# Performance work log

Measured on AMD Instinct MI355X. Metric: run time of the kernel, lower is better.

The kernel has to match this reference:

```python
import math
import jax, jax.numpy as jnp
import numpy as np

N, T, D, H, DH = 4, 2048, 1024, 16, 64
CAP = 30.0
EPS = 1e-5


def _layernorm(x, g, b):
    m = jnp.mean(x, axis=-1, keepdims=True)
    v = jnp.mean(jnp.square(x - m), axis=-1, keepdims=True)
    return (x - m) * jax.lax.rsqrt(v + EPS) * g + b


def _rope(x):
    # x: [N, H, t, d]; interleaved rotary (rotary-embedding-torch style), theta=10000
    t, d = x.shape[2], x.shape[3]
    inv_freq = 1.0 / (10000.0 ** (jnp.arange(0, d, 2, dtype=jnp.float32) / d))
    ang = jnp.arange(t, dtype=jnp.float32)[:, None] * inv_freq[None, :]  # [t, d/2]
    cos, sin = jnp.cos(ang), jnp.sin(ang)
    x1, x2 = x[..., 0::2], x[..., 1::2]
    r1 = x1 * cos - x2 * sin
    r2 = x1 * sin + x2 * cos
    return jnp.stack([r1, r2], axis=-1).reshape(x.shape)


def setup_inputs() -> dict:
    key = jax.random.key(0)
    ks = jax.random.split(key, 8)
    s = 0.02
    lengths = jax.random.randint(ks[6], (N,), T // 2, T + 1).astype(jnp.int32)
    key_padding_mask = jnp.arange(T)[None, :] >= lengths[:, None]  # True = pad
    attn_mask = jnp.triu(jnp.ones((T, T), dtype=bool), 1)  # causal: True = masked
    return {
        "x": jax.random.normal(ks[0], (N, T, D), jnp.float32),
        "ln_g": jnp.ones((D,), jnp.float32),
        "ln_b": jnp.zeros((D,), jnp.float32),
        "Wq": jax.random.normal(ks[1], (D, H * DH), jnp.float32) * s,
        "bq": jnp.zeros((H * DH,), jnp.float32),
        "Wk": jax.random.normal(ks[2], (D, H * DH), jnp.float32) * s,
        "bk": jnp.zeros((H * DH,), jnp.float32),
        "Wv": jax.random.normal(ks[3], (D, H * DH), jnp.float32) * s,
        "bv": jnp.zeros((H * DH,), jnp.float32),
        "Wo": jax.random.normal(ks[4], (H * DH, D), jnp.float32) * s,
        "bo": jnp.zeros((D,), jnp.float32),
        "key_padding_mask": key_padding_mask,
        "attn_mask": attn_mask,
        "key_value_sequence_lengths": lengths,
    }


def reference(x, ln_g, ln_b, Wq, bq, Wk, bk, Wv, bv, Wo, bo,
              key_padding_mask, attn_mask, key_value_sequence_lengths):
    n, t, _ = x.shape
    h = _layernorm(x, ln_g, ln_b)  # shared LN for q/k/v (self-attention)
    q = (h @ Wq + bq).reshape(n, t, H, DH).transpose(0, 2, 1, 3)  # [n,H,t,d]
    k = (h @ Wk + bk).reshape(n, t, H, DH).transpose(0, 2, 1, 3)
    v = (h @ Wv + bv).reshape(n, t, H, DH).transpose(0, 2, 1, 3)
    q = _rope(q)
    k = _rope(k)
    scores = jnp.einsum('bhtd,bhTd->bhtT', q, k) / math.sqrt(DH)
    scores = CAP * jnp.tanh(scores / CAP)  # tanh soft-cap
    mask = key_padding_mask[:, None, None, :] | attn_mask[None, None, :, :]
    scores = jnp.where(mask, -jnp.inf, scores)
    attn = jax.nn.softmax(scores, axis=-1)
    out = jnp.einsum('bhtT,bhTd->bhtd', attn, v)
    out = out.transpose(0, 2, 1, 3).reshape(n, t, H * DH)
    return out @ Wo + bo
```

## Files before the change

kernel.cpp:

```cpp
#include <hip/hip_runtime.h>
#include <hip/hip_bf16.h>

typedef unsigned short u16;
typedef unsigned int   u32;
typedef __bf16 bf16x8 __attribute__((ext_vector_type(8)));
typedef float  f32x4  __attribute__((ext_vector_type(4)));

#define NB 4
#define T_ 2048
#define D_ 1024
#define H_ 16
#define DH 64
#define M_ (NB * T_)
#define PSTR 72

__device__ __forceinline__ float bf2f(u16 u) {
    union { u32 i; float f; } v; v.i = ((u32)u) << 16; return v.f;
}
__device__ __forceinline__ u16 f2bf(float f) {
    union { float fl; u32 i; } v; v.fl = f;
    u32 r = v.i + 0x7fff + ((v.i >> 16) & 1);
    return (u16)(r >> 16);
}

__device__ __forceinline__ void gl_lds16(const u16* g, u16* l) {
    __builtin_amdgcn_global_load_lds((const __attribute__((address_space(1))) void*)g,
                                     (__attribute__((address_space(3))) void*)l,
                                     16, 0, 0);
}

__device__ __forceinline__ int detect_f32(const u16* p) {
    int weird = 0;
    const int lane = threadIdx.x & 63;
    #pragma unroll
    for (int i = 0; i < 4; ++i) {
        const u16 u = p[lane * 4 + i];
        const int e = (u >> 7) & 0xFF;
        weird += (e == 0xFF || (e >= 0x01 && e <= 0x3F) || (e >= 0xC0 && e <= 0xFE));
    }
    #pragma unroll
    for (int off = 32; off; off >>= 1) weird += __shfl_xor(weird, off);
    return weird >= 16;
}

__device__ __forceinline__ int read_len(const void* raw, int b) {
    const int* a32 = (const int*)raw;
    bool ok32 = true;
    #pragma unroll
    for (int i = 0; i < NB; ++i) {
        const int v = a32[i];
        if (v < 1 || v > T_) ok32 = false;
    }
    int v = ok32 ? a32[b] : (int)((const long long*)raw)[b];
    return min(max(v, 1), T_);
}

__global__ __launch_bounds__(256) void prep_kernel(const void* __restrict__ xraw,
                                                   const void* __restrict__ graw,
                                                   const void* __restrict__ braw,
                                                   u16* __restrict__ h,
                                                   const void* __restrict__ W0,
                                                   const void* __restrict__ W1,
                                                   const void* __restrict__ W2,
                                                   const void* __restrict__ W3,
                                                   u16* __restrict__ Wt0,
                                                   u16* __restrict__ Wt1,
                                                   u16* __restrict__ Wt2,
                                                   u16* __restrict__ Wt3,
                                                   float2* __restrict__ tab) {
    __shared__ __align__(16) u16 sh[64 * PSTR];
    const int bid = blockIdx.x;
    const int tid = threadIdx.x;

    if (bid < M_) {
        const int row = bid;
        const int isf = detect_f32((const u16*)xraw);
        float* red = (float*)sh;

        float xv[4];
        if (isf) {
            const float* xr = (const float*)xraw + (size_t)row * D_;
            *(float4*)xv = *(const float4*)&xr[tid * 4];
        } else {
            const u16* xr = (const u16*)xraw + (size_t)row * D_;
            u16 loc[4] __attribute__((aligned(8)));
            *(uint2*)loc = *(const uint2*)&xr[tid * 4];
            #pragma unroll
            for (int i = 0; i < 4; ++i) xv[i] = bf2f(loc[i]);
        }

        float s = xv[0] + xv[1] + xv[2] + xv[3];
        float q = xv[0]*xv[0] + xv[1]*xv[1] + xv[2]*xv[2] + xv[3]*xv[3];
        #pragma unroll
        for (int off = 32; off; off >>= 1) {
            s += __shfl_xor(s, off);
            q += __shfl_xor(q, off);
        }
        const int wave = tid >> 6, lane = tid & 63;
        if (lane == 0) { red[wave] = s; red[4 + wave] = q; }
        __syncthreads();
        s = red[0] + red[1] + red[2] + red[3];
        q = red[4] + red[5] + red[6] + red[7];

        const float mean = s * (1.0f / D_);
        const float var  = q * (1.0f / D_) - mean * mean;
        const float rs   = rsqrtf(var + 1e-5f);

        u16 o[4] __attribute__((aligned(8)));
        #pragma unroll
        for (int i = 0; i < 4; ++i) {
            const int c = tid * 4 + i;
            const float gv = isf ? ((const float*)graw)[c] : bf2f(((const u16*)graw)[c]);
            const float bv = isf ? ((const float*)braw)[c] : bf2f(((const u16*)braw)[c]);
            o[i] = f2bf((xv[i] - mean) * rs * gv + bv);
        }
        *(uint2*)&h[(size_t)row * D_ + tid * 4] = *(uint2*)o;
    } else if (bid < M_ + 1024) {
        const int w = bid - M_;
        const int z = w >> 8;
        const int t = w & 255;
        const void* Wraw = (z == 0) ? W0 : (z == 1) ? W1 : (z == 2) ? W2 : W3;
        u16* Wt          = (z == 0) ? Wt0 : (z == 1) ? Wt1 : (z == 2) ? Wt2 : Wt3;
        u16 (*tile)[PSTR] = (u16(*)[PSTR])sh;
        const int isf = detect_f32((const u16*)Wraw);
        const int n0 = (t & 15) * 64;
        const int k0 = (t >> 4) * 64;
        const int tr  = tid >> 2;
        const int tc  = (tid & 3) * 16;

        if (isf) {
            const float* W = (const float*)Wraw;
            #pragma unroll
            for (int i = 0; i < 16; ++i)
                tile[tc + i][tr] = f2bf(W[(size_t)(k0 + tr) * D_ + n0 + tc + i]);
        } else {
            const u16* W = (const u16*)Wraw;
            #pragma unroll
            for (int i = 0; i < 16; ++i)
                tile[tc + i][tr] = W[(size_t)(k0 + tr) * D_ + n0 + tc + i];
        }
        __syncthreads();
        *(uint4*)&Wt[(size_t)(n0 + tr) * D_ + k0 + tc]     = *(uint4*)&tile[tr][tc];
        *(uint4*)&Wt[(size_t)(n0 + tr) * D_ + k0 + tc + 8] = *(uint4*)&tile[tr][tc + 8];
    } else {
        const int gid = (bid - (M_ + 1024)) * 256 + tid;
        const int t = gid >> 5, i = gid & 31;
        const float inv = exp2f(-(float)i * 0.41524101186092f);
        const float ang = (float)t * inv;
        float sv, cv;
        sincosf(ang, &sv, &cv);
        tab[gid] = make_float2(cv, sv);
    }
}

__global__ __launch_bounds__(256) void wconv_kernel(const void* __restrict__ Wraw,
                                                    u16* __restrict__ Wt) {
    __shared__ u16 tile[64][PSTR];
    const int isf = detect_f32((const u16*)Wraw);
    const int n0 = blockIdx.x * 64;
    const int k0 = blockIdx.y * 64;
    const int tid = threadIdx.x;
    const int tr  = tid >> 2;
    const int tc  = (tid & 3) * 16;

    if (isf) {
        const float* W = (const float*)Wraw;
        #pragma unroll
        for (int i = 0; i < 16; ++i)
            tile[tc + i][tr] = f2bf(W[(size_t)(k0 + tr) * D_ + n0 + tc + i]);
    } else {
        const u16* W = (const u16*)Wraw;
        #pragma unroll
        for (int i = 0; i < 16; ++i)
            tile[tc + i][tr] = W[(size_t)(k0 + tr) * D_ + n0 + tc + i];
    }
    __syncthreads();
    *(uint4*)&Wt[(size_t)(n0 + tr) * D_ + k0 + tc]     = *(uint4*)&tile[tr][tc];
    *(uint4*)&Wt[(size_t)(n0 + tr) * D_ + k0 + tc + 8] = *(uint4*)&tile[tr][tc + 8];
}

__global__ __launch_bounds__(256) void vtrans_kernel(const u16* __restrict__ vtmp,
                                                     u16* __restrict__ vt) {
    __shared__ u16 tile[64][PSTR];
    const int bh = blockIdx.y;
    const int b  = bh >> 4;
    const int hh = bh & 15;
    const int t0 = blockIdx.x * 64;
    const int tid = threadIdx.x;
    const int tr  = tid >> 2;
    const int tc  = (tid & 3) * 16;

    #pragma unroll
    for (int i = 0; i < 16; ++i)
        tile[tc + i][tr] = vtmp[(size_t)(b * T_ + t0 + tr) * D_ + hh * DH + tc + i];
    __syncthreads();
    u16* dst = vt + (size_t)bh * DH * T_ + (size_t)tr * T_ + t0;
    *(uint4*)&dst[tc]     = *(uint4*)&tile[tr][tc];
    *(uint4*)&dst[tc + 8] = *(uint4*)&tile[tr][tc + 8];
}

__global__ __launch_bounds__(256) void qkv_kernel(const u16* __restrict__ A,
                                                  const u16* __restrict__ Wt3,
                                                  const void* __restrict__ Braw,
                                                  const void* __restrict__ bqr,
                                                  const void* __restrict__ bkr,
                                                  const void* __restrict__ bvr,
                                                  u16* __restrict__ qo,
                                                  u16* __restrict__ ko,
                                                  u16* __restrict__ vo,
                                                  const float2* __restrict__ tab) {
    __shared__ __align__(16) u16 As[128 * 64];
    __shared__ __align__(16) u16 Bs[128 * 64];

    const int tid   = threadIdx.x;
    const int wave  = tid >> 6;
    const int lane  = tid & 63;
    const int quad  = lane >> 4;
    const int lr    = lane & 15;

    const int bid = blockIdx.x;
    const int wg  = (bid & 7) * 192 + (bid >> 3);
    const int ntile = (wg % 24) * 128;
    const int mtile = (wg / 24) * 128;
    const int seg   = ntile >> 10;

    const int isf = detect_f32((const u16*)Braw);

    const int srow = wave * 8 + (lane >> 3);
    const int sc   = (((lane & 7) ^ (lane >> 3)) * 8);
    const u16* aP = A   + (size_t)(mtile + srow) * D_ + sc;
    const u16* bP = Wt3 + (size_t)(ntile + srow) * D_ + sc;
    u16* aL = As + (wave * 8) * 64;
    u16* bL = Bs + (wave * 8) * 64;

    const int mbase = (wave >> 1) * 64;
    const int nbase = (wave & 1) * 64;

    f32x4 acc[4][4];
    #pragma unroll
    for (int m = 0; m < 4; ++m)
        #pragma unroll
        for (int n = 0; n < 4; ++n)
            acc[m][n] = (f32x4){0.f, 0.f, 0.f, 0.f};

    for (int k0 = 0; k0 < D_; k0 += 64) {
        #pragma unroll
        for (int j = 0; j < 4; ++j) {
            gl_lds16(aP + (size_t)(j * 32) * D_ + k0, aL + (j * 32) * 64);
            gl_lds16(bP + (size_t)(j * 32) * D_ + k0, bL + (j * 32) * 64);
        }
        __syncthreads();

        #pragma unroll
        for (int c = 0; c < 2; ++c) {
            bf16x8 af[4], bfr[4];
            #pragma unroll
            for (int m = 0; m < 4; ++m) {
                const int row = mbase + m * 16 + lr;
                af[m] = *(const bf16x8*)&As[row * 64 + (((c << 2) | quad) ^ (row & 7)) * 8];
            }
            #pragma unroll
            for (int n = 0; n < 4; ++n) {
                const int row = nbase + n * 16 + lr;
                bfr[n] = *(const bf16x8*)&Bs[row * 64 + (((c << 2) | quad) ^ (row & 7)) * 8];
            }
            #pragma unroll
            for (int m = 0; m < 4; ++m)
                #pragma unroll
                for (int n = 0; n < 4; ++n)
                    acc[m][n] = __builtin_amdgcn_mfma_f32_16x16x32_bf16(af[m], bfr[n], acc[m][n], 0, 0, 0);
        }
        __syncthreads();
    }

    const void* biasraw = (seg == 0) ? bqr : (seg == 1) ? bkr : bvr;
    u16* out            = (seg == 0) ? qo  : (seg == 1) ? ko  : vo;
    const int nloc = (ntile & 1023) + nbase;

    #pragma unroll
    for (int m = 0; m < 4; ++m) {
        #pragma unroll
        for (int n = 0; n < 4; ++n) {
            const int ncl = nloc + n * 16 + lr;
            const float bv = isf ? ((const float*)biasraw)[ncl]
                                 : bf2f(((const u16*)biasraw)[ncl]);
            #pragma unroll
            for (int r = 0; r < 4; ++r) {
                const int mrow = mtile + mbase + m * 16 + quad * 4 + r;
                float v = acc[m][n][r] + bv;
                if (seg < 2) {
                    const float other = __shfl_xor(v, 1);
                    const int d = ncl & (DH - 1);
                    const int t = mrow & (T_ - 1);
                    const float2 cs = tab[t * 32 + (d >> 1)];
                    v = (d & 1) ? (other * cs.y + v * cs.x) : (v * cs.x - other * cs.y);
                }
                out[(size_t)mrow * D_ + ncl] = f2bf(v);
            }
        }
    }
}

__global__ __launch_bounds__(256) void gemm128_kernel(const u16* __restrict__ A,
                                                      const u16* __restrict__ Bt,
                                                      const void* __restrict__ Braw,
                                                      const void* __restrict__ biasraw,
                                                      void* __restrict__ out,
                                                      const int nx,
                                                      const int mode) {
    __shared__ __align__(16) u16 As[128 * 64];
    __shared__ __align__(16) u16 Bs[128 * 64];

    const int tid   = threadIdx.x;
    const int wave  = tid >> 6;
    const int lane  = tid & 63;
    const int quad  = lane >> 4;
    const int lr    = lane & 15;

    const int bid = blockIdx.x;
    const int cpx = (nx * (M_ / 128)) >> 3;
    const int wg  = (bid & 7) * cpx + (bid >> 3);
    const int ntile = (wg % nx) * 128;
    const int mtile = (wg / nx) * 128;

    const int isf = detect_f32((const u16*)Braw);

    const int srow = wave * 8 + (lane >> 3);
    const int sc   = (((lane & 7) ^ (lane >> 3)) * 8);
    const u16* aP = A  + (size_t)(mtile + srow) * D_ + sc;
    const u16* bP = Bt + (size_t)(ntile + srow) * D_ + sc;
    u16* aL = As + (wave * 8) * 64;
    u16* bL = Bs + (wave * 8) * 64;

    const int mbase = (wave >> 1) * 64;
    const int nbase = (wave & 1) * 64;

    f32x4 acc[4][4];
    #pragma unroll
    for (int m = 0; m < 4; ++m)
        #pragma unroll
        for (int n = 0; n < 4; ++n)
            acc[m][n] = (f32x4){0.f, 0.f, 0.f, 0.f};

    for (int k0 = 0; k0 < D_; k0 += 64) {
        #pragma unroll
        for (int j = 0; j < 4; ++j) {
            gl_lds16(aP + (size_t)(j * 32) * D_ + k0, aL + (j * 32) * 64);
            gl_lds16(bP + (size_t)(j * 32) * D_ + k0, bL + (j * 32) * 64);
        }
        __syncthreads();

        #pragma unroll
        for (int c = 0; c < 2; ++c) {
            bf16x8 af[4], bfr[4];
            #pragma unroll
            for (int m = 0; m < 4; ++m) {
                const int row = mbase + m * 16 + lr;
                af[m] = *(const bf16x8*)&As[row * 64 + (((c << 2) | quad) ^ (row & 7)) * 8];
            }
            #pragma unroll
            for (int n = 0; n < 4; ++n) {
                const int row = nbase + n * 16 + lr;
                bfr[n] = *(const bf16x8*)&Bs[row * 64 + (((c << 2) | quad) ^ (row & 7)) * 8];
            }
            #pragma unroll
            for (int m = 0; m < 4; ++m)
                #pragma unroll
                for (int n = 0; n < 4; ++n)
                    acc[m][n] = __builtin_amdgcn_mfma_f32_16x16x32_bf16(af[m], bfr[n], acc[m][n], 0, 0, 0);
        }
        __syncthreads();
    }

    #pragma unroll
    for (int m = 0; m < 4; ++m) {
        #pragma unroll
        for (int n = 0; n < 4; ++n) {
            const int ncol = ntile + nbase + n * 16 + lr;
            const float bv = isf ? ((const float*)biasraw)[ncol]
                                 : bf2f(((const u16*)biasraw)[ncol]);
            #pragma unroll
            for (int r = 0; r < 4; ++r) {
                const int mrow = mtile + mbase + m * 16 + quad * 4 + r;
                float v = acc[m][n][r] + bv;
                if (mode == 2) {
                    const float other = __shfl_xor(v, 1);
                    const int d = ncol & (DH - 1);
                    const int t = mrow & (T_ - 1);
                    const int i = d >> 1;
                    const float inv = exp2f(-(float)i * 0.41524101186092f);
                    const float ang = (float)t * inv;
                    float sv, cv;
                    __sincosf(ang, &sv, &cv);
                    v = (d & 1) ? (other * sv + v * cv) : (v * cv - other * sv);
                }
                const int d  = ncol & (DH - 1);
                const int hh = ncol >> 6;
                const int t  = mrow & (T_ - 1);
                const int bb = mrow >> 11;
                if (mode == 0) {
                    if (isf) ((float*)out)[(size_t)mrow * D_ + ncol] = v;
                    else     ((u16*)out)[(size_t)mrow * D_ + ncol] = f2bf(v);
                } else if (mode == 1) {
                    ((u16*)out)[(((size_t)(bb * H_ + hh) * DH) + d) * T_ + t] = f2bf(v);
                } else {
                    ((u16*)out)[(((size_t)(bb * H_ + hh) * T_) + t) * DH + d] = f2bf(v);
                }
            }
        }
    }
}

__global__ __launch_bounds__(256) void gemm_kernel(const u16* __restrict__ A,
                                                   const void* __restrict__ Braw,
                                                   const void* __restrict__ biasraw,
                                                   void* __restrict__ out,
                                                   const int mode) {
    __shared__ __align__(16) u16 As[128 * 32];
    __shared__ __align__(16) u16 Bs[64 * 32];

    const int tid   = threadIdx.x;
    const int ntile = blockIdx.x * 64;
    const int mtile = blockIdx.y * 128;
    const int wave  = tid >> 6;
    const int lane  = tid & 63;
    const int quad  = lane >> 4;
    const int lr    = lane & 15;

    const int isf = detect_f32((const u16*)Braw);
    const float* Bf = (const float*)Braw;
    const u16*   Bu = (const u16*)Braw;

    f32x4 acc[2][4];
    #pragma unroll
    for (int s = 0; s < 2; ++s)
        #pragma unroll
        for (int n = 0; n < 4; ++n)
            acc[s][n] = (f32x4){0.f, 0.f, 0.f, 0.f};

    const int ar  = tid >> 1;
    const int akb = (tid & 1) * 16;
    const int bn  = tid & 63;
    const int bkb = (tid >> 6) * 8;
    const u16* Arow = A + (size_t)(mtile + ar) * D_ + akb;
    const size_t bcol0 = (size_t)bkb * D_ + ntile + bn;

    for (int k0 = 0; k0 < D_; k0 += 32) {
        *(uint4*)&As[ar * 32 + akb]     = *(const uint4*)(Arow + k0);
        *(uint4*)&As[ar * 32 + akb + 8] = *(const uint4*)(Arow + k0 + 8);
        {
            u16 tmp[8] __attribute__((aligned(16)));
            if (isf) {
                #pragma unroll
                for (int j = 0; j < 8; ++j) tmp[j] = f2bf(Bf[bcol0 + (size_t)(k0 + j) * D_]);
            } else {
                #pragma unroll
                for (int j = 0; j < 8; ++j) tmp[j] = Bu[bcol0 + (size_t)(k0 + j) * D_];
            }
            *(uint4*)&Bs[bn * 32 + bkb] = *(uint4*)tmp;
        }
        __syncthreads();

        const int mbase = wave * 32;
        bf16x8 af0 = *(const bf16x8*)&As[(mbase +      lr) * 32 + quad * 8];
        bf16x8 af1 = *(const bf16x8*)&As[(mbase + 16 + lr) * 32 + quad * 8];
        #pragma unroll
        for (int nt = 0; nt < 4; ++nt) {
            bf16x8 bf = *(const bf16x8*)&Bs[(nt * 16 + lr) * 32 + quad * 8];
            acc[0][nt] = __builtin_amdgcn_mfma_f32_16x16x32_bf16(af0, bf, acc[0][nt], 0, 0, 0);
            acc[1][nt] = __builtin_amdgcn_mfma_f32_16x16x32_bf16(af1, bf, acc[1][nt], 0, 0, 0);
        }
        __syncthreads();
    }

    #pragma unroll
    for (int s2 = 0; s2 < 2; ++s2) {
        #pragma unroll
        for (int nt = 0; nt < 4; ++nt) {
            const int ncol = ntile + nt * 16 + lr;
            const float bv = isf ? ((const float*)biasraw)[ncol]
                                 : bf2f(((const u16*)biasraw)[ncol]);
            #pragma unroll
            for (int r = 0; r < 4; ++r) {
                const int mrow = mtile + wave * 32 + s2 * 16 + quad * 4 + r;
                float v = acc[s2][nt][r] + bv;
                if (mode == 2) {
                    const float other = __shfl_xor(v, 1);
                    const int d = ncol & (DH - 1);
                    const int t = mrow & (T_ - 1);
                    const int i = d >> 1;
                    const float inv = exp2f(-(float)i * 0.41524101186092f);
                    const float ang = (float)t * inv;
                    const float cv = cosf(ang), sv = sinf(ang);
                    v = (d & 1) ? (other * sv + v * cv) : (v * cv - other * sv);
                }
                const int d  = ncol & (DH - 1);
                const int hh = ncol >> 6;
                const int t  = mrow & (T_ - 1);
                const int bb = mrow >> 11;
                if (mode == 0) {
                    if (isf) ((float*)out)[(size_t)mrow * D_ + ncol] = v;
                    else     ((u16*)out)[(size_t)mrow * D_ + ncol] = f2bf(v);
                } else if (mode == 1) {
                    ((u16*)out)[(((size_t)(bb * H_ + hh) * DH) + d) * T_ + t] = f2bf(v);
                } else {
                    ((u16*)out)[(((size_t)(bb * H_ + hh) * T_) + t) * DH + d] = f2bf(v);
                }
            }
        }
    }
}

__global__ __launch_bounds__(256) void attn_kernel(const u16* __restrict__ Q,
                                                   const u16* __restrict__ K,
                                                   const u16* __restrict__ Vt,
                                                   const void* __restrict__ lensraw,
                                                   u16* __restrict__ ctx,
                                                   const int rowmajor) {
    __shared__ __align__(16) u16 Ps[64 * PSTR];
    __shared__ __align__(16) u16 Ps2[64 * PSTR];
    __shared__ __align__(16) u16 Ks[64 * PSTR];
    __shared__ __align__(16) u16 Vts[64 * PSTR];

    const int tid  = threadIdx.x;
    const int wave = tid >> 6;
    const int lane = tid & 63;
    const int quad = lane >> 4;
    const int lr   = lane & 15;

    const int bid = blockIdx.x;
    const int swz = (bid & 7) * 128 + (bid >> 3);
    const int qx  = swz & 15;
    const int bh  = swz >> 4;
    const int qs_lo = qx * 64;
    const int qs_hi = (31 - qx) * 64;
    const int b    = bh >> 4;
    const int hh   = bh & 15;
    const int len  = read_len(lensraw, b);

    const size_t qkstride = rowmajor ? (size_t)D_ : (size_t)DH;
    const size_t qkoff    = rowmajor ? ((size_t)b * T_ * D_ + hh * DH)
                                     : ((size_t)bh * T_ * DH);
    const u16* Qp = Q + qkoff;
    const u16* Kp = K + qkoff;
    const u16* Vb = Vt + (size_t)bh * DH * T_;

    const int srow = tid >> 2;
    const int scb  = (tid & 3) * 16;

    *(uint4*)&Ps[srow * PSTR + scb]     = *(const uint4*)&Qp[(size_t)(qs_lo + srow) * qkstride + scb];
    *(uint4*)&Ps[srow * PSTR + scb + 8] = *(const uint4*)&Qp[(size_t)(qs_lo + srow) * qkstride + scb + 8];
    const bf16x8 qaL0 = *(const bf16x8*)&Ps[(wave * 16 + lr) * PSTR + quad * 8];
    const bf16x8 qaL1 = *(const bf16x8*)&Ps[(wave * 16 + lr) * PSTR + 32 + quad * 8];
    *(uint4*)&Ps[srow * PSTR + scb]     = *(const uint4*)&Qp[(size_t)(qs_hi + srow) * qkstride + scb];
    *(uint4*)&Ps[srow * PSTR + scb + 8] = *(const uint4*)&Qp[(size_t)(qs_hi + srow) * qkstride + scb + 8];
    const bf16x8 qaH0 = *(const bf16x8*)&Ps[(wave * 16 + lr) * PSTR + quad * 8];
    const bf16x8 qaH1 = *(const bf16x8*)&Ps[(wave * 16 + lr) * PSTR + 32 + quad * 8];

    {
        uint4 k0 = *(const uint4*)&Kp[(size_t)srow * qkstride + scb];
        uint4 k1 = *(const uint4*)&Kp[(size_t)srow * qkstride + scb + 8];
        uint4 v0 = *(const uint4*)&Vb[(size_t)srow * T_ + scb];
        uint4 v1 = *(const uint4*)&Vb[(size_t)srow * T_ + scb + 8];
        *(uint4*)&Ks[srow * PSTR + scb]      = k0;
        *(uint4*)&Ks[srow * PSTR + scb + 8]  = k1;
        *(uint4*)&Vts[srow * PSTR + scb]     = v0;
        *(uint4*)&Vts[srow * PSTR + scb + 8] = v1;
    }
    __syncthreads();

    f32x4 accL[4], accH[4];
    float lL[4] = {0.f, 0.f, 0.f, 0.f};
    float lH[4] = {0.f, 0.f, 0.f, 0.f};
    #pragma unroll
    for (int nt = 0; nt < 4; ++nt) {
        accL[nt] = (f32x4){0.f, 0.f, 0.f, 0.f};
        accH[nt] = (f32x4){0.f, 0.f, 0.f, 0.f};
    }

    const int ktnL = min(qs_lo + 63, len - 1) / 64 + 1;
    const int ktnH = min(qs_hi + 63, len - 1) / 64 + 1;
    const int prow = wave * 16 + quad * 4;

    const float C1 = 1.44269504f / 120.0f;
    const float C2 = -60.0f * 1.44269504f;

    uint4 kr0, kr1, vr0, vr1;
    for (int kt = 0; kt < ktnH; ++kt) {
        const int ks = kt * 64;
        const bool havenext = (kt + 1 < ktnH);
        const bool lo_act   = (kt < ktnL);

        if (havenext) {
            const int ns = ks + 64;
            kr0 = *(const uint4*)&Kp[(size_t)(ns + srow) * qkstride + scb];
            kr1 = *(const uint4*)&Kp[(size_t)(ns + srow) * qkstride + scb + 8];
            vr0 = *(const uint4*)&Vb[(size_t)srow * T_ + ns + scb];
            vr1 = *(const uint4*)&Vb[(size_t)srow * T_ + ns + scb + 8];
        }

        f32x4 sH[4], sL[4];
        #pragma unroll
        for (int nt = 0; nt < 4; ++nt) {
            sH[nt] = (f32x4){0.f, 0.f, 0.f, 0.f};
            sL[nt] = (f32x4){0.f, 0.f, 0.f, 0.f};
        }
        __builtin_amdgcn_s_setprio(1);
        #pragma unroll
        for (int nt = 0; nt < 4; ++nt) {
            bf16x8 kb0 = *(const bf16x8*)&Ks[(nt * 16 + lr) * PSTR + quad * 8];
            bf16x8 kb1 = *(const bf16x8*)&Ks[(nt * 16 + lr) * PSTR + 32 + quad * 8];
            sH[nt] = __builtin_amdgcn_mfma_f32_16x16x32_bf16(qaH0, kb0, sH[nt], 0, 0, 0);
            sH[nt] = __builtin_amdgcn_mfma_f32_16x16x32_bf16(qaH1, kb1, sH[nt], 0, 0, 0);
            if (lo_act) {
                sL[nt] = __builtin_amdgcn_mfma_f32_16x16x32_bf16(qaL0, kb0, sL[nt], 0, 0, 0);
                sL[nt] = __builtin_amdgcn_mfma_f32_16x16x32_bf16(qaL1, kb1, sL[nt], 0, 0, 0);
            }
        }
        __builtin_amdgcn_s_setprio(0);

        {
            const bool mH = (ks == qs_hi) || (ks + 63 >= len);
            if (!mH) {
                #pragma unroll
                for (int r = 0; r < 4; ++r) {
                    #pragma unroll
                    for (int nt = 0; nt < 4; ++nt) {
                        const float z = __builtin_amdgcn_exp2f(sH[nt][r] * C1);
                        const float p = __builtin_amdgcn_exp2f(C2 * __builtin_amdgcn_rcpf(z + 1.0f));
                        lH[r] += p;
                        Ps[(prow + r) * PSTR + nt * 16 + lr] = f2bf(p);
                    }
                }
            } else {
                #pragma unroll
                for (int r = 0; r < 4; ++r) {
                    const int trow = qs_hi + prow + r;
                    #pragma unroll
                    for (int nt = 0; nt < 4; ++nt) {
                        const float z = __builtin_amdgcn_exp2f(sH[nt][r] * C1);
                        float p = __builtin_amdgcn_exp2f(C2 * __builtin_amdgcn_rcpf(z + 1.0f));
                        const int col = ks + nt * 16 + lr;
                        p = (col > trow || col >= len) ? 0.f : p;
                        lH[r] += p;
                        Ps[(prow + r) * PSTR + nt * 16 + lr] = f2bf(p);
                    }
                }
            }
        }
        if (lo_act) {
            const bool mL = (ks == qs_lo) || (ks + 63 >= len);
            if (!mL) {
                #pragma unroll
                for (int r = 0; r < 4; ++r) {
                    #pragma unroll
                    for (int nt = 0; nt < 4; ++nt) {
                        const float z = __builtin_amdgcn_exp2f(sL[nt][r] * C1);
                        const float p = __builtin_amdgcn_exp2f(C2 * __builtin_amdgcn_rcpf(z + 1.0f));
                        lL[r] += p;
                        Ps2[(prow + r) * PSTR + nt * 16 + lr] = f2bf(p);
                    }
                }
            } else {
                #pragma unroll
                for (int r = 0; r < 4; ++r) {
                    const int trow = qs_lo + prow + r;
                    #pragma unroll
                    for (int nt = 0; nt < 4; ++nt) {
                        const float z = __builtin_amdgcn_exp2f(sL[nt][r] * C1);
                        float p = __builtin_amdgcn_exp2f(C2 * __builtin_amdgcn_rcpf(z + 1.0f));
                        const int col = ks + nt * 16 + lr;
                        p = (col > trow || col >= len) ? 0.f : p;
                        lL[r] += p;
                        Ps2[(prow + r) * PSTR + nt * 16 + lr] = f2bf(p);
                    }
                }
            }
        }

        bf16x8 paH0 = *(const bf16x8*)&Ps[(wave * 16 + lr) * PSTR + quad * 8];
        bf16x8 paH1 = *(const bf16x8*)&Ps[(wave * 16 + lr) * PSTR + 32 + quad * 8];
        bf16x8 paL0 = *(const bf16x8*)&Ps2[(wave * 16 + lr) * PSTR + quad * 8];
        bf16x8 paL1 = *(const bf16x8*)&Ps2[(wave * 16 + lr) * PSTR + 32 + quad * 8];
        __builtin_amdgcn_s_setprio(1);
        #pragma unroll
        for (int nt = 0; nt < 4; ++nt) {
            bf16x8 vb0 = *(const bf16x8*)&Vts[(nt * 16 + lr) * PSTR + quad * 8];
            bf16x8 vb1 = *(const bf16x8*)&Vts[(nt * 16 + lr) * PSTR + 32 + quad * 8];
            accH[nt] = __builtin_amdgcn_mfma_f32_16x16x32_bf16(paH0, vb0, accH[nt], 0, 0, 0);
            accH[nt] = __builtin_amdgcn_mfma_f32_16x16x32_bf16(paH1, vb1, accH[nt], 0, 0, 0);
            if (lo_act) {
                accL[nt] = __builtin_amdgcn_mfma_f32_16x16x32_bf16(paL0, vb0, accL[nt], 0, 0, 0);
                accL[nt] = __builtin_amdgcn_mfma_f32_16x16x32_bf16(paL1, vb1, accL[nt], 0, 0, 0);
            }
        }
        __builtin_amdgcn_s_setprio(0);

        if (havenext) {
            __syncthreads();
            *(uint4*)&Ks[srow * PSTR + scb]      = kr0;
            *(uint4*)&Ks[srow * PSTR + scb + 8]  = kr1;
            *(uint4*)&Vts[srow * PSTR + scb]     = vr0;
            *(uint4*)&Vts[srow * PSTR + scb + 8] = vr1;
            __syncthreads();
        }
    }

    #pragma unroll
    for (int r = 0; r < 4; ++r) {
        float ll = lL[r], lh = lH[r];
        #pragma unroll
        for (int off = 1; off < 16; off <<= 1) {
            ll += __shfl_xor(ll, off);
            lh += __shfl_xor(lh, off);
        }
        const float invL = (ll > 0.f) ? (1.0f / ll) : 0.f;
        const float invH = (lh > 0.f) ? (1.0f / lh) : 0.f;
        const int qrow = prow + r;
        #pragma unroll
        for (int nt = 0; nt < 4; ++nt) {
            ctx[(size_t)(b * T_ + qs_lo + qrow) * D_ + hh * DH + nt * 16 + lr] =
                f2bf(accL[nt][r] * invL);
            ctx[(size_t)(b * T_ + qs_hi + qrow) * D_ + hh * DH + nt * 16 + lr] =
                f2bf(accH[nt][r] * invH);
        }
    }
}

extern "C" void kernel_launch(void* const* d_in, const int* in_sizes, int n_in,
                              void* d_out, int out_size, void* d_ws, size_t ws_size,
                              hipStream_t stream) {
    u16* h = (u16*)d_ws;
    const size_t MD = (size_t)M_ * D_;
    const size_t WD = (size_t)D_ * D_;
    u16* q  = h + MD;
    u16* k  = q + MD;
    u16* vt = k + MD;
    const bool havewt  = ws_size >= (4 * MD + 4 * WD) * sizeof(u16);
    const bool havebig = ws_size >= (5 * MD + 4 * WD) * sizeof(u16)
                                    + (size_t)T_ * 32 * sizeof(float2);
    u16* wtq = havewt ? (vt + MD)  : nullptr;
    u16* wtk = havewt ? (wtq + WD) : nullptr;
    u16* wtv = havewt ? (wtk + WD) : nullptr;
    u16* wto = havewt ? (wtv + WD) : nullptr;
    u16* vtmp = havebig ? (wto + WD) : nullptr;
    float2* tab = havebig ? (float2*)(vtmp + MD) : nullptr;

    if (havebig) {
        prep_kernel<<<M_ + 1024 + 256, 256, 0, stream>>>(
            d_in[0], d_in[1], d_in[2], h,
            d_in[3], d_in[5], d_in[7], d_in[9], wtq, wtk, wtv, wto, tab);

        qkv_kernel<<<1536, 256, 0, stream>>>(
            h, wtq, d_in[3], d_in[4], d_in[6], d_in[8], q, k, vtmp, tab);

        vtrans_kernel<<<dim3(T_ / 64, NB * H_), 256, 0, stream>>>(vtmp, vt);

        attn_kernel<<<(T_ / 128) * NB * H_, 256, 0, stream>>>(q, k, vt, d_in[13], h, 1);

        gemm128_kernel<<<8 * (M_ / 128), 256, 0, stream>>>(
            h, wto, d_in[9], d_in[10], d_out, 8, 0);
    } else if (havewt) {
        prep_kernel<<<M_, 256, 0, stream>>>(
            d_in[0], d_in[1], d_in[2], h,
            d_in[3], d_in[5], d_in[7], d_in[9], wtq, wtk, wtv, wto, nullptr);
        dim3 wgrid(D_ / 64, D_ / 64);
        wconv_kernel<<<wgrid, 256, 0, stream>>>(d_in[3], wtq);
        wconv_kernel<<<wgrid, 256, 0, stream>>>(d_in[5], wtk);
        wconv_kernel<<<wgrid, 256, 0, stream>>>(d_in[7], wtv);
        wconv_kernel<<<wgrid, 256, 0, stream>>>(d_in[9], wto);

        const int g1 = 8 * (M_ / 128);
        gemm128_kernel<<<g1, 256, 0, stream>>>(h, wtq, d_in[3], d_in[4], q, 8, 2);
        gemm128_kernel<<<g1, 256, 0, stream>>>(h, wtk, d_in[5], d_in[6], k, 8, 2);
        gemm128_kernel<<<g1, 256, 0, stream>>>(h, wtv, d_in[7], d_in[8], vt, 8, 1);

        attn_kernel<<<(T_ / 128) * NB * H_, 256, 0, stream>>>(q, k, vt, d_in[13], h, 0);

        gemm128_kernel<<<g1, 256, 0, stream>>>(h, wto, d_in[9], d_in[10], d_out, 8, 0);
    } else {
        prep_kernel<<<M_, 256, 0, stream>>>(
            d_in[0], d_in[1], d_in[2], h,
            d_in[3], d_in[5], d_in[7], d_in[9], nullptr, nullptr, nullptr, nullptr, nullptr);
        dim3 ggrid(D_ / 64, M_ / 128);
        gemm_kernel<<<ggrid, 256, 0, stream>>>(h, d_in[3], d_in[4], q, 2);
        gemm_kernel<<<ggrid, 256, 0, stream>>>(h, d_in[5], d_in[6], k, 2);
        gemm_kernel<<<ggrid, 256, 0, stream>>>(h, d_in[7], d_in[8], vt, 1);

        attn_kernel<<<(T_ / 128) * NB * H_, 256, 0, stream>>>(q, k, vt, d_in[13], h, 0);

        gemm_kernel<<<ggrid, 256, 0, stream>>>(h, d_in[9], d_in[10], d_out, 0);
    }
}
```

Measured before the change: 381.4 us.

## Replace paired-tile causal attention with persistent atomic work queue ordered longest-first

The attention kernel no longer pairs a low and high query tile per block to balance causal work. It now runs a persistent grid of 1024 blocks that pull single 64-row query tiles from a global atomic counter, in order from longest (highest query tile) to shortest. The counter is reset inside the prep kernel. This aims for dynamic load balancing that also accounts for varying key lengths, and drops one shared P buffer. The cost is an atomic plus an extra barrier per item, and losing the shared K/V tile reuse across two query tiles, which doubles K/V loads per unit of work.

```diff
diff --git a/kernel.cpp b/kernel.cpp
--- a/kernel.cpp
+++ b/kernel.cpp
@@ -67,7 +67,8 @@
                                                    u16* __restrict__ Wt1,
                                                    u16* __restrict__ Wt2,
                                                    u16* __restrict__ Wt3,
-                                                   float2* __restrict__ tab) {
+                                                   float2* __restrict__ tab,
+                                                   u32* __restrict__ ctr) {
     __shared__ __align__(16) u16 sh[64 * PSTR];
     const int bid = blockIdx.x;
     const int tid = threadIdx.x;
@@ -144,6 +145,7 @@
         *(uint4*)&Wt[(size_t)(n0 + tr) * D_ + k0 + tc + 8] = *(uint4*)&tile[tr][tc + 8];
     } else {
         const int gid = (bid - (M_ + 1024)) * 256 + tid;
+        if (gid == 0 && ctr) ctr[0] = 0;
         const int t = gid >> 5, i = gid & 31;
         const float inv = exp2f(-(float)i * 0.41524101186092f);
         const float ang = (float)t * inv;
@@ -516,213 +518,158 @@
                                                    const u16* __restrict__ Vt,
                                                    const void* __restrict__ lensraw,
                                                    u16* __restrict__ ctx,
+                                                   u32* __restrict__ ctr,
                                                    const int rowmajor) {
     __shared__ __align__(16) u16 Ps[64 * PSTR];
-    __shared__ __align__(16) u16 Ps2[64 * PSTR];
     __shared__ __align__(16) u16 Ks[64 * PSTR];
     __shared__ __align__(16) u16 Vts[64 * PSTR];
+    __shared__ int item_s;
 
     const int tid  = threadIdx.x;
     const int wave = tid >> 6;
     const int lane = tid & 63;
     const int quad = lane >> 4;
     const int lr   = lane & 15;
-
-    const int bid = blockIdx.x;
-    const int swz = (bid & 7) * 128 + (bid >> 3);
-    const int qx  = swz & 15;
-    const int bh  = swz >> 4;
-    const int qs_lo = qx * 64;
-    const int qs_hi = (31 - qx) * 64;
-    const int b    = bh >> 4;
-    const int hh   = bh & 15;
-    const int len  = read_len(lensraw, b);
-
-    const size_t qkstride = rowmajor ? (size_t)D_ : (size_t)DH;
-    const size_t qkoff    = rowmajor ? ((size_t)b * T_ * D_ + hh * DH)
-                                     : ((size_t)bh * T_ * DH);
-    const u16* Qp = Q + qkoff;
-    const u16* Kp = K + qkoff;
-    const u16* Vb = Vt + (size_t)bh * DH * T_;
-
     const int srow = tid >> 2;
     const int scb  = (tid & 3) * 16;
-
-    *(uint4*)&Ps[srow * PSTR + scb]     = *(const uint4*)&Qp[(size_t)(qs_lo + srow) * qkstride + scb];
-    *(uint4*)&Ps[srow * PSTR + scb + 8] = *(const uint4*)&Qp[(size_t)(qs_lo + srow) * qkstride + scb + 8];
-    const bf16x8 qaL0 = *(const bf16x8*)&Ps[(wave * 16 + lr) * PSTR + quad * 8];
-    const bf16x8 qaL1 = *(const bf16x8*)&Ps[(wave * 16 + lr) * PSTR + 32 + quad * 8];
-    *(uint4*)&Ps[srow * PSTR + scb]     = *(const uint4*)&Qp[(size_t)(qs_hi + srow) * qkstride + scb];
-    *(uint4*)&Ps[srow * PSTR + scb + 8] = *(const uint4*)&Qp[(size_t)(qs_hi + srow) * qkstride + scb + 8];
-    const bf16x8 qaH0 = *(const bf16x8*)&Ps[(wave * 16 + lr) * PSTR + quad * 8];
-    const bf16x8 qaH1 = *(const bf16x8*)&Ps[(wave * 16 + lr) * PSTR + 32 + quad * 8];
-
-    {
-        uint4 k0 = *(const uint4*)&Kp[(size_t)srow * qkstride + scb];
-        uint4 k1 = *(const uint4*)&Kp[(size_t)srow * qkstride + scb + 8];
-        uint4 v0 = *(const uint4*)&Vb[(size_t)srow * T_ + scb];
-        uint4 v1 = *(const uint4*)&Vb[(size_t)srow * T_ + scb + 8];
-        *(uint4*)&Ks[srow * PSTR + scb]      = k0;
-        *(uint4*)&Ks[srow * PSTR + scb + 8]  = k1;
-        *(uint4*)&Vts[srow * PSTR + scb]     = v0;
-        *(uint4*)&Vts[srow * PSTR + scb + 8] = v1;
-    }
-    __syncthreads();
-
-    f32x4 accL[4], accH[4];
-    float lL[4] = {0.f, 0.f, 0.f, 0.f};
-    float lH[4] = {0.f, 0.f, 0.f, 0.f};
-    #pragma unroll
-    for (int nt = 0; nt < 4; ++nt) {
-        accL[nt] = (f32x4){0.f, 0.f, 0.f, 0.f};
-        accH[nt] = (f32x4){0.f, 0.f, 0.f, 0.f};
-    }
-
-    const int ktnL = min(qs_lo + 63, len - 1) / 64 + 1;
-    const int ktnH = min(qs_hi + 63, len - 1) / 64 + 1;
     const int prow = wave * 16 + quad * 4;
 
     const float C1 = 1.44269504f / 120.0f;
     const float C2 = -60.0f * 1.44269504f;
 
-    uint4 kr0, kr1, vr0, vr1;
-    for (int kt = 0; kt < ktnH; ++kt) {
-        const int ks = kt * 64;
-        const bool havenext = (kt + 1 < ktnH);
-        const bool lo_act   = (kt < ktnL);
-
-        if (havenext) {
-            const int ns = ks + 64;
-            kr0 = *(const uint4*)&Kp[(size_t)(ns + srow) * qkstride + scb];
-            kr1 = *(const uint4*)&Kp[(size_t)(ns + srow) * qkstride + scb + 8];
-            vr0 = *(const uint4*)&Vb[(size_t)srow * T_ + ns + scb];
-            vr1 = *(const uint4*)&Vb[(size_t)srow * T_ + ns + scb + 8];
-        }
-
-        f32x4 sH[4], sL[4];
-        #pragma unroll
-        for (int nt = 0; nt < 4; ++nt) {
-            sH[nt] = (f32x4){0.f, 0.f, 0.f, 0.f};
-            sL[nt] = (f32x4){0.f, 0.f, 0.f, 0.f};
-        }
-        __builtin_amdgcn_s_setprio(1);
-        #pragma unroll
-        for (int nt = 0; nt < 4; ++nt) {
-            bf16x8 kb0 = *(const bf16x8*)&Ks[(nt * 16 + lr) * PSTR + quad * 8];
-            bf16x8 kb1 = *(const bf16x8*)&Ks[(nt * 16 + lr) * PSTR + 32 + quad * 8];
-            sH[nt] = __builtin_amdgcn_mfma_f32_16x16x32_bf16(qaH0, kb0, sH[nt], 0, 0, 0);
-            sH[nt] = __builtin_amdgcn_mfma_f32_16x16x32_bf16(qaH1, kb1, sH[nt], 0, 0, 0);
-            if (lo_act) {
-                sL[nt] = __builtin_amdgcn_mfma_f32_16x16x32_bf16(qaL0, kb0, sL[nt], 0, 0, 0);
-                sL[nt] = __builtin_amdgcn_mfma_f32_16x16x32_bf16(qaL1, kb1, sL[nt], 0, 0, 0);
-            }
-        }
-        __builtin_amdgcn_s_setprio(0);
-
+    for (int iter = 0; ; ++iter) {
+        if (tid == 0)
+            item_s = ctr ? (int)atomicAdd(ctr, 1u)
+                         : (iter == 0 ? (int)blockIdx.x : NB * H_ * 32);
+        __syncthreads();
+        const int item = item_s;
+        if (item >= NB * H_ * 32) break;
+
+        const int qt = 31 - (item >> 6);
+        const int bh = item & 63;
+        const int qs = qt * 64;
+        const int b  = bh >> 4;
+        const int hh = bh & 15;
+        const int len = read_len(lensraw, b);
+
+        const size_t qkstride = rowmajor ? (size_t)D_ : (size_t)DH;
+        const size_t qkoff    = rowmajor ? ((size_t)b * T_ * D_ + hh * DH)
+                                         : ((size_t)bh * T_ * DH);
+        const u16* Qp = Q + qkoff;
+        const u16* Kp = K + qkoff;
+        const u16* Vb = Vt + (size_t)bh * DH * T_;
+
+        *(uint4*)&Ps[srow * PSTR + scb]     = *(const uint4*)&Qp[(size_t)(qs + srow) * qkstride + scb];
+        *(uint4*)&Ps[srow * PSTR + scb + 8] = *(const uint4*)&Qp[(size_t)(qs + srow) * qkstride + scb + 8];
+        const bf16x8 qa0 = *(const bf16x8*)&Ps[(wave * 16 + lr) * PSTR + quad * 8];
+        const bf16x8 qa1 = *(const bf16x8*)&Ps[(wave * 16 + lr) * PSTR + 32 + quad * 8];
         {
-            const bool mH = (ks == qs_hi) || (ks + 63 >= len);
-            if (!mH) {
+            uint4 k0 = *(const uint4*)&Kp[(size_t)srow * qkstride + scb];
+            uint4 k1 = *(const uint4*)&Kp[(size_t)srow * qkstride + scb + 8];
+            uint4 v0 = *(const uint4*)&Vb[(size_t)srow * T_ + scb];
+            uint4 v1 = *(const uint4*)&Vb[(size_t)srow * T_ + scb + 8];
+            *(uint4*)&Ks[srow * PSTR + scb]      = k0;
+            *(uint4*)&Ks[srow * PSTR + scb + 8]  = k1;
+            *(uint4*)&Vts[srow * PSTR + scb]     = v0;
+            *(uint4*)&Vts[srow * PSTR + scb + 8] = v1;
+        }
+        __syncthreads();
+
+        f32x4 acc[4];
+        float l_loc[4] = {0.f, 0.f, 0.f, 0.f};
+        #pragma unroll
+        for (int nt = 0; nt < 4; ++nt) acc[nt] = (f32x4){0.f, 0.f, 0.f, 0.f};
+
+        const int ktn = min(qs + 63, len - 1) / 64 + 1;
+
+        uint4 kr0, kr1, vr0, vr1;
+        for (int kt = 0; kt < ktn; ++kt) {
+            const int ks = kt * 64;
+            const bool havenext = (kt + 1 < ktn);
+
+            if (havenext) {
+                const int ns = ks + 64;
+                kr0 = *(const uint4*)&Kp[(size_t)(ns + srow) * qkstride + scb];
+                kr1 = *(const uint4*)&Kp[(size_t)(ns + srow) * qkstride + scb + 8];
+                vr0 = *(const uint4*)&Vb[(size_t)srow * T_ + ns + scb];
+                vr1 = *(const uint4*)&Vb[(size_t)srow * T_ + ns + scb + 8];
+            }
+
+            f32x4 s[4];
+            #pragma unroll
+            for (int nt = 0; nt < 4; ++nt) s[nt] = (f32x4){0.f, 0.f, 0.f, 0.f};
+            __builtin_amdgcn_s_setprio(1);
+            #pragma unroll
+            for (int nt = 0; nt < 4; ++nt) {
+                bf16x8 kb0 = *(const bf16x8*)&Ks[(nt * 16 + lr) * PSTR + quad * 8];
+                bf16x8 kb1 = *(const bf16x8*)&Ks[(nt * 16 + lr) * PSTR + 32 + quad * 8];
+                s[nt] = __builtin_amdgcn_mfma_f32_16x16x32_bf16(qa0, kb0, s[nt], 0, 0, 0);
+                s[nt] = __builtin_amdgcn_mfma_f32_16x16x32_bf16(qa1, kb1, s[nt], 0, 0, 0);
+            }
+            __builtin_amdgcn_s_setprio(0);
+
+            const bool need_mask = (ks == qs) || (ks + 63 >= len);
+            if (!need_mask) {
                 #pragma unroll
                 for (int r = 0; r < 4; ++r) {
                     #pragma unroll
                     for (int nt = 0; nt < 4; ++nt) {
-                        const float z = __builtin_amdgcn_exp2f(sH[nt][r] * C1);
+                        const float z = __builtin_amdgcn_exp2f(s[nt][r] * C1);
                         const float p = __builtin_amdgcn_exp2f(C2 * __builtin_amdgcn_rcpf(z + 1.0f));
-                        lH[r] += p;
+                        l_loc[r] += p;
                         Ps[(prow + r) * PSTR + nt * 16 + lr] = f2bf(p);
                     }
                 }
             } else {
                 #pragma unroll
                 for (int r = 0; r < 4; ++r) {
-                    const int trow = qs_hi + prow + r;
+                    const int trow = qs + prow + r;
                     #pragma unroll
                     for (int nt = 0; nt < 4; ++nt) {
-                        const float z = __builtin_amdgcn_exp2f(sH[nt][r] * C1);
+                        const float z = __builtin_amdgcn_exp2f(s[nt][r] * C1);
                         float p = __builtin_amdgcn_exp2f(C2 * __builtin_amdgcn_rcpf(z + 1.0f));
                         const int col = ks + nt * 16 + lr;
                         p = (col > trow || col >= len) ? 0.f : p;
-                        lH[r] += p;
+                        l_loc[r] += p;
                         Ps[(prow + r) * PSTR + nt * 16 + lr] = f2bf(p);
                     }
                 }
             }
-        }
-        if (lo_act) {
-            const bool mL = (ks == qs_lo) || (ks + 63 >= len);
-            if (!mL) {
-                #pragma unroll
-                for (int r = 0; r < 4; ++r) {
-                    #pragma unroll
-                    for (int nt = 0; nt < 4; ++nt) {
-                        const float z = __builtin_amdgcn_exp2f(sL[nt][r] * C1);
-                        const float p = __builtin_amdgcn_exp2f(C2 * __builtin_amdgcn_rcpf(z + 1.0f));
-                        lL[r] += p;
-                        Ps2[(prow + r) * PSTR + nt * 16 + lr] = f2bf(p);
-                    }
-                }
-            } else {
-                #pragma unroll
-                for (int r = 0; r < 4; ++r) {
-                    const int trow = qs_lo + prow + r;
-                    #pragma unroll
-                    for (int nt = 0; nt < 4; ++nt) {
-                        const float z = __builtin_amdgcn_exp2f(sL[nt][r] * C1);
-                        float p = __builtin_amdgcn_exp2f(C2 * __builtin_amdgcn_rcpf(z + 1.0f));
-                        const int col = ks + nt * 16 + lr;
-                        p = (col > trow || col >= len) ? 0.f : p;
-                        lL[r] += p;
-                        Ps2[(prow + r) * PSTR + nt * 16 + lr] = f2bf(p);
-                    }
-                }
-            }
-        }
-
-        bf16x8 paH0 = *(const bf16x8*)&Ps[(wave * 16 + lr) * PSTR + quad * 8];
-        bf16x8 paH1 = *(const bf16x8*)&Ps[(wave * 16 + lr) * PSTR + 32 + quad * 8];
-        bf16x8 paL0 = *(const bf16x8*)&Ps2[(wave * 16 + lr) * PSTR + quad * 8];
-        bf16x8 paL1 = *(const bf16x8*)&Ps2[(wave * 16 + lr) * PSTR + 32 + quad * 8];
-        __builtin_amdgcn_s_setprio(1);
-        #pragma unroll
-        for (int nt = 0; nt < 4; ++nt) {
-            bf16x8 vb0 = *(const bf16x8*)&Vts[(nt * 16 + lr) * PSTR + quad * 8];
-            bf16x8 vb1 = *(const bf16x8*)&Vts[(nt * 16 + lr) * PSTR + 32 + quad * 8];
-            accH[nt] = __builtin_amdgcn_mfma_f32_16x16x32_bf16(paH0, vb0, accH[nt], 0, 0, 0);
-            accH[nt] = __builtin_amdgcn_mfma_f32_16x16x32_bf16(paH1, vb1, accH[nt], 0, 0, 0);
-            if (lo_act) {
-                accL[nt] = __builtin_amdgcn_mfma_f32_16x16x32_bf16(paL0, vb0, accL[nt], 0, 0, 0);
-                accL[nt] = __builtin_amdgcn_mfma_f32_16x16x32_bf16(paL1, vb1, accL[nt], 0, 0, 0);
-            }
-        }
-        __builtin_amdgcn_s_setprio(0);
-
-        if (havenext) {
-            __syncthreads();
-            *(uint4*)&Ks[srow * PSTR + scb]      = kr0;
-            *(uint4*)&Ks[srow * PSTR + scb + 8]  = kr1;
-            *(uint4*)&Vts[srow * PSTR + scb]     = vr0;
-            *(uint4*)&Vts[srow * PSTR + scb + 8] = vr1;
-            __syncthreads();
-        }
-    }
-
-    #pragma unroll
-    for (int r = 0; r < 4; ++r) {
-        float ll = lL[r], lh = lH[r];
-        #pragma unroll
-        for (int off = 1; off < 16; off <<= 1) {
-            ll += __shfl_xor(ll, off);
-            lh += __shfl_xor(lh, off);
-        }
-        const float invL = (ll > 0.f) ? (1.0f / ll) : 0.f;
-        const float invH = (lh > 0.f) ? (1.0f / lh) : 0.f;
-        const int qrow = prow + r;
-        #pragma unroll
-        for (int nt = 0; nt < 4; ++nt) {
-            ctx[(size_t)(b * T_ + qs_lo + qrow) * D_ + hh * DH + nt * 16 + lr] =
-                f2bf(accL[nt][r] * invL);
-            ctx[(size_t)(b * T_ + qs_hi + qrow) * D_ + hh * DH + nt * 16 + lr] =
-                f2bf(accH[nt][r] * invH);
+
+            bf16x8 pa0 = *(const bf16x8*)&Ps[(wave * 16 + lr) * PSTR + quad * 8];
+            bf16x8 pa1 = *(const bf16x8*)&Ps[(wave * 16 + lr) * PSTR + 32 + quad * 8];
+            __builtin_amdgcn_s_setprio(1);
+            #pragma unroll
+            for (int nt = 0; nt < 4; ++nt) {
+                bf16x8 vb0 = *(const bf16x8*)&Vts[(nt * 16 + lr) * PSTR + quad * 8];
+                bf16x8 vb1 = *(const bf16x8*)&Vts[(nt * 16 + lr) * PSTR + 32 + quad * 8];
+                acc[nt] = __builtin_amdgcn_mfma_f32_16x16x32_bf16(pa0, vb0, acc[nt], 0, 0, 0);
+                acc[nt] = __builtin_amdgcn_mfma_f32_16x16x32_bf16(pa1, vb1, acc[nt], 0, 0, 0);
+            }
+            __builtin_amdgcn_s_setprio(0);
+
+            if (havenext) {
+                __syncthreads();
+                *(uint4*)&Ks[srow * PSTR + scb]      = kr0;
+                *(uint4*)&Ks[srow * PSTR + scb + 8]  = kr1;
+                *(uint4*)&Vts[srow * PSTR + scb]     = vr0;
+                *(uint4*)&Vts[srow * PSTR + scb + 8] = vr1;
+                __syncthreads();
+            }
+        }
+
+        #pragma unroll
+        for (int r = 0; r < 4; ++r) {
+            float l = l_loc[r];
+            #pragma unroll
+            for (int off = 1; off < 16; off <<= 1) l += __shfl_xor(l, off);
+            const float invl = (l > 0.f) ? (1.0f / l) : 0.f;
+            const int qrow = prow + r;
+            #pragma unroll
+            for (int nt = 0; nt < 4; ++nt) {
+                ctx[(size_t)(b * T_ + qs + qrow) * D_ + hh * DH + nt * 16 + lr] =
+                    f2bf(acc[nt][r] * invl);
+            }
         }
     }
 }
@@ -738,32 +685,33 @@
     u16* vt = k + MD;
     const bool havewt  = ws_size >= (4 * MD + 4 * WD) * sizeof(u16);
     const bool havebig = ws_size >= (5 * MD + 4 * WD) * sizeof(u16)
-                                    + (size_t)T_ * 32 * sizeof(float2);
+                                    + (size_t)T_ * 32 * sizeof(float2) + 64;
     u16* wtq = havewt ? (vt + MD)  : nullptr;
     u16* wtk = havewt ? (wtq + WD) : nullptr;
     u16* wtv = havewt ? (wtk + WD) : nullptr;
     u16* wto = havewt ? (wtv + WD) : nullptr;
     u16* vtmp = havebig ? (wto + WD) : nullptr;
     float2* tab = havebig ? (float2*)(vtmp + MD) : nullptr;
+    u32* ctr = havebig ? (u32*)(tab + (size_t)T_ * 32) : nullptr;
 
     if (havebig) {
         prep_kernel<<<M_ + 1024 + 256, 256, 0, stream>>>(
             d_in[0], d_in[1], d_in[2], h,
-            d_in[3], d_in[5], d_in[7], d_in[9], wtq, wtk, wtv, wto, tab);
+            d_in[3], d_in[5], d_in[7], d_in[9], wtq, wtk, wtv, wto, tab, ctr);
 
         qkv_kernel<<<1536, 256, 0, stream>>>(
             h, wtq, d_in[3], d_in[4], d_in[6], d_in[8], q, k, vtmp, tab);
 
         vtrans_kernel<<<dim3(T_ / 64, NB * H_), 256, 0, stream>>>(vtmp, vt);
 
-        attn_kernel<<<(T_ / 128) * NB * H_, 256, 0, stream>>>(q, k, vt, d_in[13], h, 1);
+        attn_kernel<<<1024, 256, 0, stream>>>(q, k, vt, d_in[13], h, ctr, 1);
 
         gemm128_kernel<<<8 * (M_ / 128), 256, 0, stream>>>(
             h, wto, d_in[9], d_in[10], d_out, 8, 0);
     } else if (havewt) {
         prep_kernel<<<M_, 256, 0, stream>>>(
             d_in[0], d_in[1], d_in[2], h,
-            d_in[3], d_in[5], d_in[7], d_in[9], wtq, wtk, wtv, wto, nullptr);
+            d_in[3], d_in[5], d_in[7], d_in[9], wtq, wtk, wtv, wto, nullptr, nullptr);
         dim3 wgrid(D_ / 64, D_ / 64);
         wconv_kernel<<<wgrid, 256, 0, stream>>>(d_in[3], wtq);
         wconv_kernel<<<wgrid, 256, 0, stream>>>(d_in[5], wtk);
@@ -775,19 +723,19 @@
         gemm128_kernel<<<g1, 256, 0, stream>>>(h, wtk, d_in[5], d_in[6], k, 8, 2);
         gemm128_kernel<<<g1, 256, 0, stream>>>(h, wtv, d_in[7], d_in[8], vt, 8, 1);
 
-        attn_kernel<<<(T_ / 128) * NB * H_, 256, 0, stream>>>(q, k, vt, d_in[13], h, 0);
+        attn_kernel<<<NB * H_ * 32, 256, 0, stream>>>(q, k, vt, d_in[13], h, nullptr, 0);
 
         gemm128_kernel<<<g1, 256, 0, stream>>>(h, wto, d_in[9], d_in[10], d_out, 8, 0);
     } else {
         prep_kernel<<<M_, 256, 0, stream>>>(
             d_in[0], d_in[1], d_in[2], h,
-            d_in[3], d_in[5], d_in[7], d_in[9], nullptr, nullptr, nullptr, nullptr, nullptr);
+            d_in[3], d_in[5], d_in[7], d_in[9], nullptr, nullptr, nullptr, nullptr, nullptr, nullptr);
         dim3 ggrid(D_ / 64, M_ / 128);
         gemm_kernel<<<ggrid, 256, 0, stream>>>(h, d_in[3], d_in[4], q, 2);
         gemm_kernel<<<ggrid, 256, 0, stream>>>(h, d_in[5], d_in[6], k, 2);
         gemm_kernel<<<ggrid, 256, 0, stream>>>(h, d_in[7], d_in[8], vt, 1);
 
-        attn_kernel<<<(T_ / 128) * NB * H_, 256, 0, stream>>>(q, k, vt, d_in[13], h, 0);
+        attn_kernel<<<NB * H_ * 32, 256, 0, stream>>>(q, k, vt, d_in[13], h, nullptr, 0);
 
         gemm_kernel<<<ggrid, 256, 0, stream>>>(h, d_in[9], d_in[10], d_out, 0);
     }
```

New measurement: 360.5 us. 5.5% less time.
